# Performance work log

Hardware: AMD Instinct MI355X
Metric: run time of the kernel (lower is better)

The kernel has to match this reference:

```python
import jax, jax.numpy as jnp
import numpy as np
from jax import lax

NEG = -10000.0
NTAGS = 27
START, STOP = 25, 26


def setup_inputs() -> dict:
    key = jax.random.key(0)
    ks = jax.random.split(key, 14)
    V, T, E, H = 200000, 8192, 100, 256
    sent = jax.random.randint(ks[0], (1, T), 0, V)
    attention_mask = jnp.ones((1, T), dtype=jnp.int32)
    emb = jax.random.normal(ks[1], (V, E), jnp.float32)
    s = 1.0 / np.sqrt(H)  # torch LSTM/Linear default init bound
    u = lambda k, shape: jax.random.uniform(k, shape, jnp.float32, -s, s)
    w_ih0 = u(ks[2], (4 * H, E)); w_hh0 = u(ks[3], (4 * H, H))
    b_ih0 = u(ks[4], (4 * H,)); b_hh0 = u(ks[5], (4 * H,))
    w_ih1 = u(ks[6], (4 * H, H)); w_hh1 = u(ks[7], (4 * H, H))
    b_ih1 = u(ks[8], (4 * H,)); b_hh1 = u(ks[9], (4 * H,))
    w_lin = u(ks[10], (NTAGS, H)); b_lin = u(ks[11], (NTAGS,))
    transitions = jax.random.uniform(ks[12], (NTAGS, NTAGS), jnp.float32, 0.0, 1.0)
    transitions = (transitions.at[:, START].set(NEG)
                               .at[STOP, :].set(NEG)
                               .at[START, STOP].set(NEG))
    return dict(sent=sent, attention_mask=attention_mask, emb=emb,
                w_ih0=w_ih0, w_hh0=w_hh0, b_ih0=b_ih0, b_hh0=b_hh0,
                w_ih1=w_ih1, w_hh1=w_hh1, b_ih1=b_ih1, b_hh1=b_hh1,
                w_lin=w_lin, b_lin=b_lin, transitions=transitions)


def _lstm_layer(x, w_ih, w_hh, b_ih, b_hh):
    # x: [T, in]; torch gate order i, f, g, o
    H = w_hh.shape[1]
    xp = x @ w_ih.T + (b_ih + b_hh)  # [T, 4H], precompute input projection

    def step(carry, xt):
        h, c = carry
        g = xt + w_hh @ h
        i, f, gg, o = jnp.split(g, 4)
        i = jax.nn.sigmoid(i); f = jax.nn.sigmoid(f)
        gg = jnp.tanh(gg); o = jax.nn.sigmoid(o)
        c = f * c + i * gg
        h = o * jnp.tanh(c)
        return (h, c), h

    z = jnp.zeros((H,), x.dtype)
    _, hs = lax.scan(step, (z, z), xp)
    return hs  # [T, H]


def _viterbi(scores, mask, transitions):
    # scores: [T, 27]; mask: [T] bool. Masked steps are identity (state and
    # backpointer pass-through), matching decoding only over the valid prefix.
    v0 = jnp.full((NTAGS,), NEG, scores.dtype).at[START].set(0.0)
    idt = jnp.arange(NTAGS)

    def step(v, inp):
        emit, m = inp
        sc = v[:, None] + transitions          # [from, to]
        bp = jnp.argmax(sc, axis=0)            # best previous tag per next tag
        vn = jnp.max(sc, axis=0) + emit
        return jnp.where(m, vn, v), jnp.where(m, bp, idt)

    vT, bptrs = lax.scan(step, v0, (scores, mask))
    term = vT + transitions[:, STOP]
    best = jnp.argmax(term)
    path_score = term[best]

    def back(tag, bp):
        return bp[tag], tag

    _, path = lax.scan(back, best, bptrs, reverse=True)  # path[t] = best tag at t
    return path_score, path


def reference(sent, attention_mask, emb, w_ih0, w_hh0, b_ih0, b_hh0,
              w_ih1, w_hh1, b_ih1, b_hh1, w_lin, b_lin, transitions):
    x = emb[sent[0]]                                   # [T, 100]
    x = _lstm_layer(x, w_ih0, w_hh0, b_ih0, b_hh0)     # [T, 256]
    x = _lstm_layer(x, w_ih1, w_hh1, b_ih1, b_hh1)     # [T, 256]
    scores = x @ w_lin.T + b_lin                       # [T, 27] emission scores
    mask = attention_mask[0].astype(bool)
    path_score, path = _viterbi(scores, mask, transitions)
    return path_score, path
```

## Files before the change

kernel.cpp:

```cpp
#include <hip/hip_runtime.h>
#include <math.h>

#define SEQT 8192
#define HID  256
#define NTG  27
#define NEGV -10000.0f
#define START_TAG 25
#define STOP_TAG  26
#define T0B 16
#define T1B 32
#define VITBLK (T0B + T1B)
#define NBLKS  (T0B + T1B + 1)

__device__ __forceinline__ float agent_load(const float* p) {
  return __hip_atomic_load(const_cast<float*>(p), __ATOMIC_RELAXED, __HIP_MEMORY_SCOPE_AGENT);
}
__device__ __forceinline__ void agent_store(float* p, float v) {
  __hip_atomic_store(p, v, __ATOMIC_RELAXED, __HIP_MEMORY_SCOPE_AGENT);
}
__device__ __forceinline__ float poll_val(const float* p, int* dead) {
  float v = agent_load(p);
  if (fabsf(v) < 2.0f) return v;
  if (*dead) return 0.0f;
  int ctr = 0;
  while (true) {
    __builtin_amdgcn_s_sleep(1);
    v = agent_load(p);
    if (fabsf(v) < 2.0f) return v;
    if (++ctr > (1 << 22)) { *dead = 1; return 0.0f; }
  }
}
__device__ __forceinline__ float sigm(float x) { return 1.0f / (1.0f + __expf(-x)); }
__device__ __forceinline__ float tanh_f(float x) {
  x = fminf(15.0f, fmaxf(-15.0f, x));
  float e = __expf(-2.0f * x);
  return (1.0f - e) / (1.0f + e);
}

__device__ void team0_run(int kb, const int* sent, const float* emb,
                          const float* w_ih0, const float* w_hh0,
                          const float* b_ih0, const float* b_hh0,
                          float* h0hist) {
  __shared__ float hb[8 * 36];
  __shared__ float xb[2][8 * 20];
  __shared__ float part[512];
  __shared__ float preact[64];
  __shared__ int   deadf;

  const int tid = threadIdx.x;
  const int rl  = tid & 63;
  const int qc  = tid >> 6;
  const int grow = (rl >> 4) * 256 + kb * 16 + (rl & 15);

  float wh[32];
#pragma unroll
  for (int j = 0; j < 32; ++j) wh[j] = w_hh0[grow * 256 + qc * 32 + j];
  float wx[16];
#pragma unroll
  for (int j = 0; j < 16; ++j) {
    int c = qc * 16 + j;
    wx[j] = (c < 100) ? w_ih0[grow * 100 + c] : 0.0f;
  }
  float bsum = 0.0f, cst = 0.0f;
  if (tid < 64) bsum = b_ih0[grow] + b_hh0[grow];
  if (tid == 0) deadf = 0;

  if (tid >= 448) {
    int lane = tid - 448;
    int s0 = sent[0];
    for (int e = lane; e < 128; e += 64) {
      float v = (e < 100) ? emb[s0 * 100 + e] : 0.0f;
      xb[0][(e >> 4) * 20 + (e & 15)] = v;
    }
  }
  __syncthreads();

  for (int t = 0; t < SEQT; ++t) {
    const int par = t & 1;
    if (tid >= 256) {
      int i = tid - 256;
      float v = (t == 0) ? 0.0f : poll_val(h0hist + (t - 1) * HID + i, &deadf);
      hb[(i >> 5) * 36 + (i & 31)] = v;
    }
    __syncthreads();
    float acc = 0.0f;
    {
      const float4* h4 = (const float4*)(hb + qc * 36);
      const float4* x4 = (const float4*)(xb[par] + qc * 20);
#pragma unroll
      for (int m = 0; m < 8; ++m) {
        float4 h = h4[m];
        acc += wh[4*m+0]*h.x + wh[4*m+1]*h.y + wh[4*m+2]*h.z + wh[4*m+3]*h.w;
      }
#pragma unroll
      for (int m = 0; m < 4; ++m) {
        float4 x = x4[m];
        acc += wx[4*m+0]*x.x + wx[4*m+1]*x.y + wx[4*m+2]*x.z + wx[4*m+3]*x.w;
      }
    }
    part[tid] = acc;
    if (tid >= 448 && t + 1 < SEQT) {
      int lane = tid - 448;
      int s0 = sent[t + 1];
      for (int e = lane; e < 128; e += 64) {
        float v = (e < 100) ? emb[s0 * 100 + e] : 0.0f;
        xb[par ^ 1][(e >> 4) * 20 + (e & 15)] = v;
      }
    }
    __syncthreads();
    if (tid < 64) {
      float s = bsum;
#pragma unroll
      for (int q = 0; q < 8; ++q) s += part[q * 64 + tid];
      preact[tid] = s;
    }
    __syncthreads();
    if (tid < 16) {
      float gi = sigm(preact[tid]);
      float gf = sigm(preact[16 + tid]);
      float gg = tanh_f(preact[32 + tid]);
      float go = sigm(preact[48 + tid]);
      cst = gf * cst + gi * gg;
      float h = go * tanh_f(cst);
      agent_store(h0hist + t * HID + kb * 16 + tid, h);
    }
  }
}

__device__ void team1_run(int kb, const float* w_ih1, const float* w_hh1,
                          const float* b_ih1, const float* b_hh1,
                          const float* h0hist, float* h1hist) {
  __shared__ float hb[16 * 36];
  __shared__ float part[512];
  __shared__ float preact[32];
  __shared__ int   deadf;

  const int tid = threadIdx.x;
  const int rl  = tid & 31;
  const int qc  = tid >> 5;
  const int grow = (rl >> 3) * 256 + kb * 8 + (rl & 7);

  float wc[32];
#pragma unroll
  for (int j = 0; j < 32; ++j) {
    int c = qc * 32 + j;
    wc[j] = (c < 256) ? w_ih1[grow * 256 + c] : w_hh1[grow * 256 + (c - 256)];
  }
  float bsum = 0.0f, cst = 0.0f;
  if (tid < 32) bsum = b_ih1[grow] + b_hh1[grow];
  if (tid == 0) deadf = 0;
  __syncthreads();

  for (int t = 0; t < SEQT; ++t) {
    {
      float v;
      if (tid < 256) v = poll_val(h0hist + t * HID + tid, &deadf);
      else v = (t == 0) ? 0.0f : poll_val(h1hist + (t - 1) * HID + (tid - 256), &deadf);
      hb[(tid >> 5) * 36 + (tid & 31)] = v;
    }
    __syncthreads();
    float acc = 0.0f;
    {
      const float4* h4 = (const float4*)(hb + qc * 36);
#pragma unroll
      for (int m = 0; m < 8; ++m) {
        float4 h = h4[m];
        acc += wc[4*m+0]*h.x + wc[4*m+1]*h.y + wc[4*m+2]*h.z + wc[4*m+3]*h.w;
      }
    }
    part[tid] = acc;
    __syncthreads();
    if (tid < 32) {
      float s = bsum;
#pragma unroll
      for (int q = 0; q < 16; ++q) s += part[q * 32 + tid];
      preact[tid] = s;
    }
    __syncthreads();
    if (tid < 8) {
      float gi = sigm(preact[tid]);
      float gf = sigm(preact[8 + tid]);
      float gg = tanh_f(preact[16 + tid]);
      float go = sigm(preact[24 + tid]);
      cst = gf * cst + gi * gg;
      float h = go * tanh_f(cst);
      agent_store(h1hist + t * HID + kb * 8 + tid, h);
    }
  }
}

__device__ void viterbi_run(const int* amask, const float* w_lin, const float* b_lin,
                            const float* trans, const float* h1hist,
                            int* bp, float* out) {
  __shared__ float hb[8 * 36];
  __shared__ float spart[216];
  __shared__ float vbuf[NTG];
  __shared__ int   maps[128][NTG];
  __shared__ int   btag[129];
  __shared__ int   deadf;

  const int tid  = threadIdx.x;
  const int lane = tid & 63;
  const int stag = tid / 8, sq = tid % 8;

  float ws[32];
  if (tid < 216) {
#pragma unroll
    for (int j = 0; j < 32; ++j) ws[j] = w_lin[stag * 256 + sq * 32 + j];
  }
  float tcol[NTG]; float vreg = 0.0f, blin = 0.0f, tstop = 0.0f;
  if (tid < NTG) {
#pragma unroll
    for (int f = 0; f < NTG; ++f) tcol[f] = trans[f * NTG + tid];
    tstop = trans[tid * NTG + STOP_TAG];
    blin  = b_lin[tid];
    vreg  = (tid == START_TAG) ? 0.0f : NEGV;
    vbuf[tid] = vreg;
  }
  if (tid == 0) deadf = 0;
  float emit = 0.0f;
  __syncthreads();

  for (int it = 0; it <= SEQT; ++it) {
    if (tid >= 256 && it < SEQT) {
      int i = tid - 256;
      float v = poll_val(h1hist + it * HID + i, &deadf);
      hb[(i >> 5) * 36 + (i & 31)] = v;
    }
    if (tid < NTG && it >= 1) {
      int tm1 = it - 1;
      int m = amask[tm1];
      float vf[NTG];
#pragma unroll
      for (int f = 0; f < NTG; ++f) vf[f] = vbuf[f];
      float best = -3.0e38f; int bpi = 0;
#pragma unroll
      for (int f = 0; f < NTG; ++f) {
        float c = vf[f] + tcol[f];
        if (c > best) { best = c; bpi = f; }
      }
      float vn   = best + emit;
      float vnew = m ? vn : vreg;
      int   bpv  = m ? bpi : tid;
      vreg = vnew;
      vbuf[tid] = vnew;
      bp[tm1 * NTG + tid] = bpv;
    }
    __syncthreads();
    if (tid < 216 && it < SEQT) {
      const float4* h4 = (const float4*)(hb + sq * 36);
      float acc = 0.0f;
#pragma unroll
      for (int m = 0; m < 8; ++m) {
        float4 h = h4[m];
        acc += ws[4*m+0]*h.x + ws[4*m+1]*h.y + ws[4*m+2]*h.z + ws[4*m+3]*h.w;
      }
      spart[tid] = acc;
    }
    __syncthreads();
    if (tid < NTG && it < SEQT) {
      float s = blin;
#pragma unroll
      for (int q = 0; q < 8; ++q) s += spart[tid * 8 + q];
      emit = s;
    }
  }
  __syncthreads();

  if (tid < 64) {
    float tv = (lane < NTG) ? (vbuf[lane] + tstop) : -3.0e38f;
    int   ti = (lane < NTG) ? lane : NTG;
#pragma unroll
    for (int off = 32; off >= 1; off >>= 1) {
      float ov = __shfl_xor(tv, off);
      int   oi = __shfl_xor(ti, off);
      if ((ov > tv) || (ov == tv && oi < ti)) { tv = ov; ti = oi; }
    }
    if (lane == 0) { out[0] = tv; btag[128] = ti; }
  }
  __syncthreads();

  {
    int bs[7], es[7], tg[7], nk = 0;
#pragma unroll
    for (int k = 0; k < 7; ++k) {
      int task = tid + k * 512;
      if (task < 128 * NTG) { bs[k] = task / NTG; es[k] = task % NTG; tg[k] = es[k]; nk = k + 1; }
      else { bs[k] = 0; es[k] = 0; tg[k] = 0; }
    }
    for (int i = 63; i >= 0; --i) {
#pragma unroll
      for (int k = 0; k < 7; ++k)
        if (k < nk) tg[k] = bp[(bs[k] * 64 + i) * NTG + tg[k]];
    }
#pragma unroll
    for (int k = 0; k < 7; ++k) if (k < nk) maps[bs[k]][es[k]] = tg[k];
  }
  __syncthreads();

  if (tid == 0) {
    int e = btag[128];
    for (int b = 127; b >= 0; --b) { btag[b] = e; e = maps[b][e]; }
  }
  __syncthreads();

  if (tid < 128) {
    int b = tid, tag = btag[b];
    for (int i = 63; i >= 0; --i) {
      out[1 + b * 64 + i] = (float)tag;
      tag = bp[(b * 64 + i) * NTG + tag];
    }
  }
}

__global__ __launch_bounds__(512, 1)
void lstm_crf_kernel(const int* sent, const int* amask, const float* emb,
                     const float* w_ih0, const float* w_hh0,
                     const float* b_ih0, const float* b_hh0,
                     const float* w_ih1, const float* w_hh1,
                     const float* b_ih1, const float* b_hh1,
                     const float* w_lin, const float* b_lin, const float* trans,
                     float* h0hist, float* h1hist, int* bp, float* out) {
  int b = blockIdx.x;
  if (b < T0B)       team0_run(b, sent, emb, w_ih0, w_hh0, b_ih0, b_hh0, h0hist);
  else if (b < VITBLK) team1_run(b - T0B, w_ih1, w_hh1, b_ih1, b_hh1, h0hist, h1hist);
  else               viterbi_run(amask, w_lin, b_lin, trans, h1hist, bp, out);
}

extern "C" void kernel_launch(void* const* d_in, const int* in_sizes, int n_in,
                              void* d_out, int out_size, void* d_ws, size_t ws_size,
                              hipStream_t stream) {
  const int*   sent  = (const int*)d_in[0];
  const int*   amask = (const int*)d_in[1];
  const float* emb   = (const float*)d_in[2];
  const float* w_ih0 = (const float*)d_in[3];
  const float* w_hh0 = (const float*)d_in[4];
  const float* b_ih0 = (const float*)d_in[5];
  const float* b_hh0 = (const float*)d_in[6];
  const float* w_ih1 = (const float*)d_in[7];
  const float* w_hh1 = (const float*)d_in[8];
  const float* b_ih1 = (const float*)d_in[9];
  const float* b_hh1 = (const float*)d_in[10];
  const float* w_lin = (const float*)d_in[11];
  const float* b_lin = (const float*)d_in[12];
  const float* trans = (const float*)d_in[13];

  float* h0hist = (float*)d_ws;
  float* h1hist = h0hist + (size_t)SEQT * HID;
  int*   bp     = (int*)(h1hist + (size_t)SEQT * HID);
  float* out    = (float*)d_out;

  (void)hipMemsetAsync(d_ws, 0x7F, (size_t)2 * SEQT * HID * sizeof(float), stream);

  lstm_crf_kernel<<<NBLKS, 512, 0, stream>>>(
      sent, amask, emb, w_ih0, w_hh0, b_ih0, b_hh0,
      w_ih1, w_hh1, b_ih1, b_hh1, w_lin, b_lin, trans,
      h0hist, h1hist, bp, out);
}
```

Measured before the change: 18.15 ms.

## Restructure LSTM-CRF pipeline into per-wavefront workers without block barriers

Replaces the block-level teams, which needed several __syncthreads per timestep, with independent 64-lane wavefronts. Each wavefront owns four hidden cells, holds its weights in registers, polls the previous hidden state directly from global memory and reduces gates with lane shuffles. Emission scores now come from a separate block that writes a scores buffer, and the Viterbi recursion runs on a single wavefront using shuffles and byte-sized backpointers. The aim is to remove barrier and shared-memory latency from the serial critical path. In exchange there is more global polling traffic, and the wait loops now time out silently instead of setting a dead flag.

```diff
diff --git a/kernel.cpp b/kernel.cpp
--- a/kernel.cpp
+++ b/kernel.cpp
@@ -7,28 +7,18 @@
 #define NEGV -10000.0f
 #define START_TAG 25
 #define STOP_TAG  26
-#define T0B 16
-#define T1B 32
-#define VITBLK (T0B + T1B)
-#define NBLKS  (T0B + T1B + 1)
+#define POLL_LIM  (1 << 21)
+
+#define L1_BASE 8
+#define EM_BLK  16
+#define CRF_BLK 17
+#define NBLKS   18
 
 __device__ __forceinline__ float agent_load(const float* p) {
   return __hip_atomic_load(const_cast<float*>(p), __ATOMIC_RELAXED, __HIP_MEMORY_SCOPE_AGENT);
 }
 __device__ __forceinline__ void agent_store(float* p, float v) {
   __hip_atomic_store(p, v, __ATOMIC_RELAXED, __HIP_MEMORY_SCOPE_AGENT);
-}
-__device__ __forceinline__ float poll_val(const float* p, int* dead) {
-  float v = agent_load(p);
-  if (fabsf(v) < 2.0f) return v;
-  if (*dead) return 0.0f;
-  int ctr = 0;
-  while (true) {
-    __builtin_amdgcn_s_sleep(1);
-    v = agent_load(p);
-    if (fabsf(v) < 2.0f) return v;
-    if (++ctr > (1 << 22)) { *dead = 1; return 0.0f; }
-  }
 }
 __device__ __forceinline__ float sigm(float x) { return 1.0f / (1.0f + __expf(-x)); }
 __device__ __forceinline__ float tanh_f(float x) {
@@ -37,239 +27,256 @@
   return (1.0f - e) / (1.0f + e);
 }
 
-__device__ void team0_run(int kb, const int* sent, const float* emb,
-                          const float* w_ih0, const float* w_hh0,
-                          const float* b_ih0, const float* b_hh0,
-                          float* h0hist) {
-  __shared__ float hb[8 * 36];
-  __shared__ float xb[2][8 * 20];
-  __shared__ float part[512];
-  __shared__ float preact[64];
-  __shared__ int   deadf;
-
+__device__ void l0_run(int wid, const int* sent, const float* emb,
+                       const float* w_ih0, const float* w_hh0,
+                       const float* b_ih0, const float* b_hh0,
+                       float* h0hist) {
+  const int lane = threadIdx.x & 63;
+  const int g = lane >> 4, r = lane & 15;
+  const int cb = wid * 4;
+
+  float wh[4][16], wx[4][7];
+#pragma unroll
+  for (int j = 0; j < 4; ++j) {
+    const int row = g * 256 + cb + j;
+#pragma unroll
+    for (int k = 0; k < 16; ++k) wh[j][k] = w_hh0[row * 256 + k * 16 + r];
+#pragma unroll
+    for (int m = 0; m < 7; ++m) {
+      int c = m * 16 + r;
+      wx[j][m] = (c < 100) ? w_ih0[row * 100 + c] : 0.0f;
+    }
+  }
+  float bI = 0, bF = 0, bG = 0, bO = 0, cst = 0.0f;
+  if (lane < 4) {
+    int cell = cb + lane;
+    bI = b_ih0[cell]       + b_hh0[cell];
+    bF = b_ih0[256 + cell] + b_hh0[256 + cell];
+    bG = b_ih0[512 + cell] + b_hh0[512 + cell];
+    bO = b_ih0[768 + cell] + b_hh0[768 + cell];
+  }
+
+  for (int t = 0; t < SEQT; ++t) {
+    float xv[7];
+    {
+      const int s = sent[t];
+      const float* xrow = emb + (size_t)s * 100;
+#pragma unroll
+      for (int m = 0; m < 7; ++m) {
+        int c = m * 16 + r;
+        xv[m] = (c < 100) ? xrow[c] : 0.0f;
+      }
+    }
+    float hv[16];
+    if (t > 0) {
+      const float* hp = h0hist + (size_t)(t - 1) * HID + r;
+      int ctr = 0, ok;
+      do {
+        ok = 1;
+#pragma unroll
+        for (int k = 0; k < 16; ++k) {
+          hv[k] = agent_load(hp + k * 16);
+          ok &= (fabsf(hv[k]) < 2.0f);
+        }
+      } while (!ok && ++ctr < POLL_LIM);
+    } else {
+#pragma unroll
+      for (int k = 0; k < 16; ++k) hv[k] = 0.0f;
+    }
+    float acc[4] = {0.f, 0.f, 0.f, 0.f};
+#pragma unroll
+    for (int m = 0; m < 7; ++m)
+#pragma unroll
+      for (int j = 0; j < 4; ++j) acc[j] = fmaf(wx[j][m], xv[m], acc[j]);
+#pragma unroll
+    for (int k = 0; k < 16; ++k)
+#pragma unroll
+      for (int j = 0; j < 4; ++j) acc[j] = fmaf(wh[j][k], hv[k], acc[j]);
+#pragma unroll
+    for (int d = 1; d < 16; d <<= 1)
+#pragma unroll
+      for (int j = 0; j < 4; ++j) acc[j] += __shfl_xor(acc[j], d);
+    float v = (r == 0) ? acc[0] : (r == 1) ? acc[1] : (r == 2) ? acc[2] : acc[3];
+    float gI = __shfl(v, lane);
+    float gF = __shfl(v, 16 + lane);
+    float gG = __shfl(v, 32 + lane);
+    float gO = __shfl(v, 48 + lane);
+    if (lane < 4) {
+      float gi = sigm(gI + bI), gf = sigm(gF + bF);
+      float gg = tanh_f(gG + bG), go = sigm(gO + bO);
+      cst = gf * cst + gi * gg;
+      agent_store(h0hist + (size_t)t * HID + cb + lane, go * tanh_f(cst));
+    }
+  }
+}
+
+__device__ void l1_run(int wid, const float* w_ih1, const float* w_hh1,
+                       const float* b_ih1, const float* b_hh1,
+                       const float* h0hist, float* h1hist) {
+  const int lane = threadIdx.x & 63;
+  const int g = lane >> 4, r = lane & 15;
+  const int cb = wid * 4;
+
+  float wx[4][16], wh[4][16];
+#pragma unroll
+  for (int j = 0; j < 4; ++j) {
+    const int row = g * 256 + cb + j;
+#pragma unroll
+    for (int k = 0; k < 16; ++k) {
+      wx[j][k] = w_ih1[row * 256 + k * 16 + r];
+      wh[j][k] = w_hh1[row * 256 + k * 16 + r];
+    }
+  }
+  float bI = 0, bF = 0, bG = 0, bO = 0, cst = 0.0f;
+  if (lane < 4) {
+    int cell = cb + lane;
+    bI = b_ih1[cell]       + b_hh1[cell];
+    bF = b_ih1[256 + cell] + b_hh1[256 + cell];
+    bG = b_ih1[512 + cell] + b_hh1[512 + cell];
+    bO = b_ih1[768 + cell] + b_hh1[768 + cell];
+  }
+
+  for (int t = 0; t < SEQT; ++t) {
+    float x0[16];
+    {
+      const float* hp = h0hist + (size_t)t * HID + r;
+      int ctr = 0, ok;
+      do {
+        ok = 1;
+#pragma unroll
+        for (int k = 0; k < 16; ++k) {
+          x0[k] = agent_load(hp + k * 16);
+          ok &= (fabsf(x0[k]) < 2.0f);
+        }
+      } while (!ok && ++ctr < POLL_LIM);
+    }
+    const float* hp1 = h1hist + (size_t)(t - 1) * HID + r;
+    float hv[16];
+    if (t > 0) {
+#pragma unroll
+      for (int k = 0; k < 16; ++k) hv[k] = agent_load(hp1 + k * 16);
+    } else {
+#pragma unroll
+      for (int k = 0; k < 16; ++k) hv[k] = 0.0f;
+    }
+    float acc[4] = {0.f, 0.f, 0.f, 0.f};
+#pragma unroll
+    for (int k = 0; k < 16; ++k)
+#pragma unroll
+      for (int j = 0; j < 4; ++j) acc[j] = fmaf(wx[j][k], x0[k], acc[j]);
+    if (t > 0) {
+      int ctr = 0;
+      for (;;) {
+        int ok = 1;
+#pragma unroll
+        for (int k = 0; k < 16; ++k) ok &= (fabsf(hv[k]) < 2.0f);
+        if (ok || ++ctr >= POLL_LIM) break;
+#pragma unroll
+        for (int k = 0; k < 16; ++k) hv[k] = agent_load(hp1 + k * 16);
+      }
+    }
+#pragma unroll
+    for (int k = 0; k < 16; ++k)
+#pragma unroll
+      for (int j = 0; j < 4; ++j) acc[j] = fmaf(wh[j][k], hv[k], acc[j]);
+#pragma unroll
+    for (int d = 1; d < 16; d <<= 1)
+#pragma unroll
+      for (int j = 0; j < 4; ++j) acc[j] += __shfl_xor(acc[j], d);
+    float v = (r == 0) ? acc[0] : (r == 1) ? acc[1] : (r == 2) ? acc[2] : acc[3];
+    float gI = __shfl(v, lane);
+    float gF = __shfl(v, 16 + lane);
+    float gG = __shfl(v, 32 + lane);
+    float gO = __shfl(v, 48 + lane);
+    if (lane < 4) {
+      float gi = sigm(gI + bI), gf = sigm(gF + bF);
+      float gg = tanh_f(gG + bG), go = sigm(gO + bO);
+      cst = gf * cst + gi * gg;
+      agent_store(h1hist + (size_t)t * HID + cb + lane, go * tanh_f(cst));
+    }
+  }
+}
+
+__device__ void em_run(int wv, const float* w_lin, const float* b_lin,
+                       const float* h1hist, float* scores) {
+  const int lane = threadIdx.x & 63;
+  const int tp = lane >> 1, h = lane & 1;
+  const int tq = (tp < NTG) ? tp : NTG - 1;
+  const bool active = (tp < NTG);
+
+  float wl[128];
+#pragma unroll
+  for (int c = 0; c < 128; ++c) wl[c] = w_lin[tq * 256 + h * 128 + c];
+  const float bl = b_lin[tq] + 1000.0f;
+
+  for (int t = wv; t < SEQT; t += 8) {
+    const float* hp = h1hist + (size_t)t * HID + h * 128;
+    float acc;
+    int ctr = 0, ok;
+    do {
+      ok = 1; acc = 0.0f;
+#pragma unroll
+      for (int c = 0; c < 128; ++c) {
+        float v = agent_load(hp + c);
+        ok &= (fabsf(v) < 2.0f);
+        acc = fmaf(wl[c], v, acc);
+      }
+    } while (!ok && ++ctr < POLL_LIM);
+    acc += __shfl_xor(acc, 1);
+    if (active && h == 0) agent_store(scores + t * 32 + tp, acc + bl);
+  }
+}
+
+__device__ void crf_run(const int* amask, const float* trans,
+                        const float* scores, unsigned char* bpb, float* out) {
+  __shared__ int btag[129];
+  __shared__ int maps[128][NTG];
   const int tid = threadIdx.x;
-  const int rl  = tid & 63;
-  const int qc  = tid >> 6;
-  const int grow = (rl >> 4) * 256 + kb * 16 + (rl & 15);
-
-  float wh[32];
-#pragma unroll
-  for (int j = 0; j < 32; ++j) wh[j] = w_hh0[grow * 256 + qc * 32 + j];
-  float wx[16];
-#pragma unroll
-  for (int j = 0; j < 16; ++j) {
-    int c = qc * 16 + j;
-    wx[j] = (c < 100) ? w_ih0[grow * 100 + c] : 0.0f;
-  }
-  float bsum = 0.0f, cst = 0.0f;
-  if (tid < 64) bsum = b_ih0[grow] + b_hh0[grow];
-  if (tid == 0) deadf = 0;
-
-  if (tid >= 448) {
-    int lane = tid - 448;
-    int s0 = sent[0];
-    for (int e = lane; e < 128; e += 64) {
-      float v = (e < 100) ? emb[s0 * 100 + e] : 0.0f;
-      xb[0][(e >> 4) * 20 + (e & 15)] = v;
-    }
-  }
-  __syncthreads();
-
-  for (int t = 0; t < SEQT; ++t) {
-    const int par = t & 1;
-    if (tid >= 256) {
-      int i = tid - 256;
-      float v = (t == 0) ? 0.0f : poll_val(h0hist + (t - 1) * HID + i, &deadf);
-      hb[(i >> 5) * 36 + (i & 31)] = v;
-    }
-    __syncthreads();
-    float acc = 0.0f;
-    {
-      const float4* h4 = (const float4*)(hb + qc * 36);
-      const float4* x4 = (const float4*)(xb[par] + qc * 20);
-#pragma unroll
-      for (int m = 0; m < 8; ++m) {
-        float4 h = h4[m];
-        acc += wh[4*m+0]*h.x + wh[4*m+1]*h.y + wh[4*m+2]*h.z + wh[4*m+3]*h.w;
-      }
-#pragma unroll
-      for (int m = 0; m < 4; ++m) {
-        float4 x = x4[m];
-        acc += wx[4*m+0]*x.x + wx[4*m+1]*x.y + wx[4*m+2]*x.z + wx[4*m+3]*x.w;
-      }
-    }
-    part[tid] = acc;
-    if (tid >= 448 && t + 1 < SEQT) {
-      int lane = tid - 448;
-      int s0 = sent[t + 1];
-      for (int e = lane; e < 128; e += 64) {
-        float v = (e < 100) ? emb[s0 * 100 + e] : 0.0f;
-        xb[par ^ 1][(e >> 4) * 20 + (e & 15)] = v;
-      }
-    }
-    __syncthreads();
-    if (tid < 64) {
-      float s = bsum;
-#pragma unroll
-      for (int q = 0; q < 8; ++q) s += part[q * 64 + tid];
-      preact[tid] = s;
-    }
-    __syncthreads();
-    if (tid < 16) {
-      float gi = sigm(preact[tid]);
-      float gf = sigm(preact[16 + tid]);
-      float gg = tanh_f(preact[32 + tid]);
-      float go = sigm(preact[48 + tid]);
-      cst = gf * cst + gi * gg;
-      float h = go * tanh_f(cst);
-      agent_store(h0hist + t * HID + kb * 16 + tid, h);
-    }
-  }
-}
-
-__device__ void team1_run(int kb, const float* w_ih1, const float* w_hh1,
-                          const float* b_ih1, const float* b_hh1,
-                          const float* h0hist, float* h1hist) {
-  __shared__ float hb[16 * 36];
-  __shared__ float part[512];
-  __shared__ float preact[32];
-  __shared__ int   deadf;
-
-  const int tid = threadIdx.x;
-  const int rl  = tid & 31;
-  const int qc  = tid >> 5;
-  const int grow = (rl >> 3) * 256 + kb * 8 + (rl & 7);
-
-  float wc[32];
-#pragma unroll
-  for (int j = 0; j < 32; ++j) {
-    int c = qc * 32 + j;
-    wc[j] = (c < 256) ? w_ih1[grow * 256 + c] : w_hh1[grow * 256 + (c - 256)];
-  }
-  float bsum = 0.0f, cst = 0.0f;
-  if (tid < 32) bsum = b_ih1[grow] + b_hh1[grow];
-  if (tid == 0) deadf = 0;
-  __syncthreads();
-
-  for (int t = 0; t < SEQT; ++t) {
-    {
-      float v;
-      if (tid < 256) v = poll_val(h0hist + t * HID + tid, &deadf);
-      else v = (t == 0) ? 0.0f : poll_val(h1hist + (t - 1) * HID + (tid - 256), &deadf);
-      hb[(tid >> 5) * 36 + (tid & 31)] = v;
-    }
-    __syncthreads();
-    float acc = 0.0f;
-    {
-      const float4* h4 = (const float4*)(hb + qc * 36);
-#pragma unroll
-      for (int m = 0; m < 8; ++m) {
-        float4 h = h4[m];
-        acc += wc[4*m+0]*h.x + wc[4*m+1]*h.y + wc[4*m+2]*h.z + wc[4*m+3]*h.w;
-      }
-    }
-    part[tid] = acc;
-    __syncthreads();
-    if (tid < 32) {
-      float s = bsum;
-#pragma unroll
-      for (int q = 0; q < 16; ++q) s += part[q * 32 + tid];
-      preact[tid] = s;
-    }
-    __syncthreads();
-    if (tid < 8) {
-      float gi = sigm(preact[tid]);
-      float gf = sigm(preact[8 + tid]);
-      float gg = tanh_f(preact[16 + tid]);
-      float go = sigm(preact[24 + tid]);
-      cst = gf * cst + gi * gg;
-      float h = go * tanh_f(cst);
-      agent_store(h1hist + t * HID + kb * 8 + tid, h);
-    }
-  }
-}
-
-__device__ void viterbi_run(const int* amask, const float* w_lin, const float* b_lin,
-                            const float* trans, const float* h1hist,
-                            int* bp, float* out) {
-  __shared__ float hb[8 * 36];
-  __shared__ float spart[216];
-  __shared__ float vbuf[NTG];
-  __shared__ int   maps[128][NTG];
-  __shared__ int   btag[129];
-  __shared__ int   deadf;
-
-  const int tid  = threadIdx.x;
-  const int lane = tid & 63;
-  const int stag = tid / 8, sq = tid % 8;
-
-  float ws[32];
-  if (tid < 216) {
-#pragma unroll
-    for (int j = 0; j < 32; ++j) ws[j] = w_lin[stag * 256 + sq * 32 + j];
-  }
-  float tcol[NTG]; float vreg = 0.0f, blin = 0.0f, tstop = 0.0f;
-  if (tid < NTG) {
-#pragma unroll
-    for (int f = 0; f < NTG; ++f) tcol[f] = trans[f * NTG + tid];
-    tstop = trans[tid * NTG + STOP_TAG];
-    blin  = b_lin[tid];
-    vreg  = (tid == START_TAG) ? 0.0f : NEGV;
-    vbuf[tid] = vreg;
-  }
-  if (tid == 0) deadf = 0;
-  float emit = 0.0f;
-  __syncthreads();
-
-  for (int it = 0; it <= SEQT; ++it) {
-    if (tid >= 256 && it < SEQT) {
-      int i = tid - 256;
-      float v = poll_val(h1hist + it * HID + i, &deadf);
-      hb[(i >> 5) * 36 + (i & 31)] = v;
-    }
-    if (tid < NTG && it >= 1) {
-      int tm1 = it - 1;
-      int m = amask[tm1];
-      float vf[NTG];
-#pragma unroll
-      for (int f = 0; f < NTG; ++f) vf[f] = vbuf[f];
-      float best = -3.0e38f; int bpi = 0;
-#pragma unroll
-      for (int f = 0; f < NTG; ++f) {
-        float c = vf[f] + tcol[f];
-        if (c > best) { best = c; bpi = f; }
-      }
-      float vn   = best + emit;
-      float vnew = m ? vn : vreg;
-      int   bpv  = m ? bpi : tid;
-      vreg = vnew;
-      vbuf[tid] = vnew;
-      bp[tm1 * NTG + tid] = bpv;
-    }
-    __syncthreads();
-    if (tid < 216 && it < SEQT) {
-      const float4* h4 = (const float4*)(hb + sq * 36);
-      float acc = 0.0f;
-#pragma unroll
-      for (int m = 0; m < 8; ++m) {
-        float4 h = h4[m];
-        acc += ws[4*m+0]*h.x + ws[4*m+1]*h.y + ws[4*m+2]*h.z + ws[4*m+3]*h.w;
-      }
-      spart[tid] = acc;
-    }
-    __syncthreads();
-    if (tid < NTG && it < SEQT) {
-      float s = blin;
-#pragma unroll
-      for (int q = 0; q < 8; ++q) s += spart[tid * 8 + q];
-      emit = s;
-    }
-  }
-  __syncthreads();
-
-  if (tid < 64) {
-    float tv = (lane < NTG) ? (vbuf[lane] + tstop) : -3.0e38f;
-    int   ti = (lane < NTG) ? lane : NTG;
+
+  if ((tid >> 6) == 0) {
+    const int lane = tid & 63;
+    const int tau = lane & 31, half = lane >> 5;
+    const bool act = (tau < NTG);
+    const int tq = act ? tau : NTG - 1;
+
+    float tc[14];
+#pragma unroll
+    for (int k = 0; k < 14; ++k) {
+      int f = half ? (13 + k) : k;
+      tc[k] = trans[f * NTG + tq];
+    }
+    const float tstop = trans[tq * NTG + STOP_TAG];
+    float vreg = (act && tau == START_TAG) ? 0.0f : NEGV;
+
+    for (int t = 0; t < SEQT; ++t) {
+      float e = 0.0f;
+      if (act) {
+        const float* sp = scores + t * 32 + tau;
+        int ctr = 0;
+        e = agent_load(sp);
+        while (e >= 2000.0f && ++ctr < POLL_LIM) e = agent_load(sp);
+        e -= 1000.0f;
+      }
+      const int m = amask[t];
+      float best = -3.0e38f; int barg = 0;
+#pragma unroll
+      for (int k = 0; k < 14; ++k) {
+        int f = half ? (13 + k) : k;
+        float vf = __shfl(vreg, half ? (45 + k) : k);
+        float c = vf + tc[k];
+        if (c > best) { best = c; barg = f; }
+      }
+      float ob = __shfl_xor(best, 32);
+      int   oa = __shfl_xor(barg, 32);
+      bool take = half ? (ob >= best) : (ob > best);
+      if (take) { best = ob; barg = oa; }
+      float vn = best + e;
+      vreg = m ? vn : vreg;
+      int bpv = m ? barg : tau;
+      if (act && half == 0) bpb[(t << 5) + tau] = (unsigned char)bpv;
+    }
+    float tv = (act && half == 0) ? (vreg + tstop) : -3.0e38f;
+    int   ti = (act && half == 0) ? tau : 64;
 #pragma unroll
     for (int off = 32; off >= 1; off >>= 1) {
       float ov = __shfl_xor(tv, off);
@@ -291,7 +298,7 @@
     for (int i = 63; i >= 0; --i) {
 #pragma unroll
       for (int k = 0; k < 7; ++k)
-        if (k < nk) tg[k] = bp[(bs[k] * 64 + i) * NTG + tg[k]];
+        if (k < nk) tg[k] = bpb[((bs[k] * 64 + i) << 5) + tg[k]];
     }
 #pragma unroll
     for (int k = 0; k < 7; ++k) if (k < nk) maps[bs[k]][es[k]] = tg[k];
@@ -308,23 +315,31 @@
     int b = tid, tag = btag[b];
     for (int i = 63; i >= 0; --i) {
       out[1 + b * 64 + i] = (float)tag;
-      tag = bp[(b * 64 + i) * NTG + tag];
+      tag = bpb[((b * 64 + i) << 5) + tag];
     }
   }
 }
 
 __global__ __launch_bounds__(512, 1)
-void lstm_crf_kernel(const int* sent, const int* amask, const float* emb,
-                     const float* w_ih0, const float* w_hh0,
-                     const float* b_ih0, const float* b_hh0,
-                     const float* w_ih1, const float* w_hh1,
-                     const float* b_ih1, const float* b_hh1,
-                     const float* w_lin, const float* b_lin, const float* trans,
-                     float* h0hist, float* h1hist, int* bp, float* out) {
-  int b = blockIdx.x;
-  if (b < T0B)       team0_run(b, sent, emb, w_ih0, w_hh0, b_ih0, b_hh0, h0hist);
-  else if (b < VITBLK) team1_run(b - T0B, w_ih1, w_hh1, b_ih1, b_hh1, h0hist, h1hist);
-  else               viterbi_run(amask, w_lin, b_lin, trans, h1hist, bp, out);
+void lstm_crf_pipeline(const int* sent, const int* amask, const float* emb,
+                       const float* w_ih0, const float* w_hh0,
+                       const float* b_ih0, const float* b_hh0,
+                       const float* w_ih1, const float* w_hh1,
+                       const float* b_ih1, const float* b_hh1,
+                       const float* w_lin, const float* b_lin, const float* trans,
+                       float* h0hist, float* h1hist, float* scores,
+                       unsigned char* bpb, float* out) {
+  const int b = blockIdx.x;
+  const int wv = threadIdx.x >> 6;
+  if (b < L1_BASE) {
+    l0_run(b * 8 + wv, sent, emb, w_ih0, w_hh0, b_ih0, b_hh0, h0hist);
+  } else if (b < EM_BLK) {
+    l1_run((b - L1_BASE) * 8 + wv, w_ih1, w_hh1, b_ih1, b_hh1, h0hist, h1hist);
+  } else if (b == EM_BLK) {
+    em_run(wv, w_lin, b_lin, h1hist, scores);
+  } else {
+    crf_run(amask, trans, scores, bpb, out);
+  }
 }
 
 extern "C" void kernel_launch(void* const* d_in, const int* in_sizes, int n_in,
@@ -347,13 +362,16 @@
 
   float* h0hist = (float*)d_ws;
   float* h1hist = h0hist + (size_t)SEQT * HID;
-  int*   bp     = (int*)(h1hist + (size_t)SEQT * HID);
-  float* out    = (float*)d_out;
-
-  (void)hipMemsetAsync(d_ws, 0x7F, (size_t)2 * SEQT * HID * sizeof(float), stream);
-
-  lstm_crf_kernel<<<NBLKS, 512, 0, stream>>>(
+  float* scores = h1hist + (size_t)SEQT * HID;
+  unsigned char* bpb = (unsigned char*)(scores + (size_t)SEQT * 32);
+  float* out = (float*)d_out;
+
+  (void)hipMemsetAsync(d_ws, 0x7F,
+                       ((size_t)2 * SEQT * HID + (size_t)SEQT * 32) * sizeof(float),
+                       stream);
+
+  lstm_crf_pipeline<<<NBLKS, 512, 0, stream>>>(
       sent, amask, emb, w_ih0, w_hh0, b_ih0, b_hh0,
       w_ih1, w_hh1, b_ih1, b_hh1, w_lin, b_lin, trans,
-      h0hist, h1hist, bp, out);
-}
+      h0hist, h1hist, scores, bpb, out);
+}
```

New measurement: 19.46 ms. 1.07x slower.
